# Kernel tuning notes

Measured on AMD Instinct MI355X. Metric: run time of the kernel, lower is better.

## Reference

```python
import jax, jax.numpy as jnp
import numpy as np

B = 64        # number of bags
D = 512       # feature dim
T = 131072    # total instances across all bags (ragged, avg ~2048/bag)


def setup_inputs() -> dict:
    key = jax.random.key(0)
    k_s, _ = jax.random.split(key)
    samples = jax.random.normal(k_s, (T, D), dtype=jnp.float32)
    # Ragged bag sizes that sum exactly to T (deterministic).
    rng = np.random.default_rng(0)
    w = rng.random(B)
    counts = np.floor(w / w.sum() * T).astype(np.int64)
    counts = np.maximum(counts, 1)
    counts[-1] += T - counts.sum()
    bags_num_samples = jnp.asarray(counts, dtype=jnp.int64)
    return {"samples": samples, "bags_num_samples": bags_num_samples}


def reference(samples, bags_num_samples):
    # Fused segmented mean-pool replacing the per-bag Python loop:
    # bag i owns rows [cum[i-1], cum[i]) of `samples`.
    n_bags = bags_num_samples.shape[0]
    total = samples.shape[0]
    seg_ids = jnp.repeat(jnp.arange(n_bags), bags_num_samples,
                         total_repeat_length=total)  # [T]
    sums = jax.ops.segment_sum(samples, seg_ids, num_segments=n_bags)  # [B, D]
    return sums / bags_num_samples[:, None].astype(samples.dtype)
```

## Files before the change

kernel.cpp:

```cpp
#include <hip/hip_runtime.h>

#define NBAGS 64
#define D 512
#define D4 128
#define TARGET_CHUNKS 1024
#define GRID1 1088


__device__ __forceinline__ int lane_incl_scan(int v, int lane) {
#pragma unroll
    for (int off = 1; off < 64; off <<= 1) {
        int o = __shfl_up(v, off, 64);
        if (lane >= off) v += o;
    }
    return v;
}

__global__ __launch_bounds__(256) void
agg_partial_kernel(const float* __restrict__ samples,
                   const int* __restrict__ counts,
                   float* __restrict__ partials, int tt) {
    __shared__ int s_bag, s_r0, s_r1;
    const int t = threadIdx.x;
    const int g = blockIdx.x;

    if (t == 0) s_bag = -1;
    if (t < 64) {
        const int c = counts[t];
        int n = (c * TARGET_CHUNKS) / tt;
        if (n < 1) n = 1;
        int S = n;
#pragma unroll
        for (int m = 1; m < 64; m <<= 1) S += __shfl_xor(S, m, 64);
        int L = TARGET_CHUNKS - S; if (L < 0) L = 0;
        n += (t < L) ? 1 : 0;
        const int cb = lane_incl_scan(n, t) - n;
        const int rb = lane_incl_scan(c, t) - c;
        if (g >= cb && g < cb + n) {
            const int j = g - cb;
            s_bag = t;
            s_r0 = rb + (c * j) / n;
            s_r1 = rb + (c * (j + 1)) / n;
        }
    }
    __syncthreads();
    if (s_bag < 0) return;
    const int r0 = s_r0, r1 = s_r1;

    const int col  = t & (D4 - 1);
    const int half = t >> 7;

    const float4* __restrict__ src = (const float4*)samples;

    float4 a0 = make_float4(0.f, 0.f, 0.f, 0.f);
    float4 a1 = make_float4(0.f, 0.f, 0.f, 0.f);
    int r = r0 + half;
    for (; r + 6 < r1; r += 8) {
        float4 v0 = src[(r    ) * D4 + col];
        float4 v1 = src[(r + 2) * D4 + col];
        float4 v2 = src[(r + 4) * D4 + col];
        float4 v3 = src[(r + 6) * D4 + col];
        a0.x += v0.x; a0.y += v0.y; a0.z += v0.z; a0.w += v0.w;
        a1.x += v1.x; a1.y += v1.y; a1.z += v1.z; a1.w += v1.w;
        a0.x += v2.x; a0.y += v2.y; a0.z += v2.z; a0.w += v2.w;
        a1.x += v3.x; a1.y += v3.y; a1.z += v3.z; a1.w += v3.w;
    }
    for (; r < r1; r += 2) {
        float4 v = src[r * D4 + col];
        a0.x += v.x; a0.y += v.y; a0.z += v.z; a0.w += v.w;
    }
    a0.x += a1.x; a0.y += a1.y; a0.z += a1.z; a0.w += a1.w;

    __shared__ float4 lds[D4];
    if (half == 1) lds[col] = a0;
    __syncthreads();
    if (half == 0) {
        float4 o = lds[col];
        a0.x += o.x; a0.y += o.y; a0.z += o.z; a0.w += o.w;
        ((float4*)partials)[g * D4 + col] = a0;
    }
}

__global__ __launch_bounds__(D4) void
agg_reduce_kernel(const float* __restrict__ partials,
                  const int* __restrict__ counts,
                  float* __restrict__ out, int tt) {
    __shared__ int s_cb, s_n;
    const int t   = threadIdx.x;
    const int bag = blockIdx.x;

    if (t < 64) {
        const int c = counts[t];
        int n = (c * TARGET_CHUNKS) / tt;
        if (n < 1) n = 1;
        int S = n;
#pragma unroll
        for (int m = 1; m < 64; m <<= 1) S += __shfl_xor(S, m, 64);
        int L = TARGET_CHUNKS - S; if (L < 0) L = 0;
        n += (t < L) ? 1 : 0;
        const int cb = lane_incl_scan(n, t) - n;
        if (t == bag) { s_cb = cb; s_n = n; }
    }
    __syncthreads();
    const int cb = s_cb, n = s_n;

    const float4* __restrict__ p = (const float4*)partials;
    float4 acc = make_float4(0.f, 0.f, 0.f, 0.f);
    for (int k = 0; k < n; ++k) {
        float4 v = p[(cb + k) * D4 + t];
        acc.x += v.x; acc.y += v.y; acc.z += v.z; acc.w += v.w;
    }
    const float inv = 1.0f / (float)counts[bag];
    acc.x *= inv; acc.y *= inv; acc.z *= inv; acc.w *= inv;
    ((float4*)out)[bag * D4 + t] = acc;
}

extern "C" void kernel_launch(void* const* d_in, const int* in_sizes, int n_in,
                              void* d_out, int out_size, void* d_ws, size_t ws_size,
                              hipStream_t stream) {
    const float* samples  = (const float*)d_in[0];
    const int*   counts   = (const int*)d_in[1];
    float*       out      = (float*)d_out;
    float*       partials = (float*)d_ws;
    const int    tt       = in_sizes[0] / D;

    agg_partial_kernel<<<GRID1, 256, 0, stream>>>(samples, counts, partials, tt);
    agg_reduce_kernel<<<NBAGS, D4, 0, stream>>>(partials, counts, out, tt);
}
```

Measured before the change: 56.21 us.

## Fuse partial and reduce kernels using atomicAdd into zeroed output

Drops the second reduction kernel and the partials workspace. Each chunk block now scales its partial sum by 1/count and atomically adds it into the output, which is zeroed first with hipMemsetAsync. This removes one kernel launch and the partials write/read round trip, at the cost of float atomics, a memset launch, and non-deterministic summation order.

```diff
diff --git a/kernel.cpp b/kernel.cpp
--- a/kernel.cpp
+++ b/kernel.cpp
@@ -17,10 +17,10 @@
 }
 
 __global__ __launch_bounds__(256) void
-agg_partial_kernel(const float* __restrict__ samples,
-                   const int* __restrict__ counts,
-                   float* __restrict__ partials, int tt) {
-    __shared__ int s_bag, s_r0, s_r1;
+agg_fused_kernel(const float* __restrict__ samples,
+                 const int* __restrict__ counts,
+                 float* __restrict__ out, int tt) {
+    __shared__ int s_bag, s_r0, s_r1, s_cnt;
     const int t = threadIdx.x;
     const int g = blockIdx.x;
 
@@ -39,6 +39,7 @@
         if (g >= cb && g < cb + n) {
             const int j = g - cb;
             s_bag = t;
+            s_cnt = c;
             s_r0 = rb + (c * j) / n;
             s_r1 = rb + (c * (j + 1)) / n;
         }
@@ -77,53 +78,23 @@
     if (half == 0) {
         float4 o = lds[col];
         a0.x += o.x; a0.y += o.y; a0.z += o.z; a0.w += o.w;
-        ((float4*)partials)[g * D4 + col] = a0;
+        const float inv = 1.0f / (float)s_cnt;
+        float* dst = out + s_bag * D + col * 4;
+        atomicAdd(dst + 0, a0.x * inv);
+        atomicAdd(dst + 1, a0.y * inv);
+        atomicAdd(dst + 2, a0.z * inv);
+        atomicAdd(dst + 3, a0.w * inv);
     }
-}
-
-__global__ __launch_bounds__(D4) void
-agg_reduce_kernel(const float* __restrict__ partials,
-                  const int* __restrict__ counts,
-                  float* __restrict__ out, int tt) {
-    __shared__ int s_cb, s_n;
-    const int t   = threadIdx.x;
-    const int bag = blockIdx.x;
-
-    if (t < 64) {
-        const int c = counts[t];
-        int n = (c * TARGET_CHUNKS) / tt;
-        if (n < 1) n = 1;
-        int S = n;
-#pragma unroll
-        for (int m = 1; m < 64; m <<= 1) S += __shfl_xor(S, m, 64);
-        int L = TARGET_CHUNKS - S; if (L < 0) L = 0;
-        n += (t < L) ? 1 : 0;
-        const int cb = lane_incl_scan(n, t) - n;
-        if (t == bag) { s_cb = cb; s_n = n; }
-    }
-    __syncthreads();
-    const int cb = s_cb, n = s_n;
-
-    const float4* __restrict__ p = (const float4*)partials;
-    float4 acc = make_float4(0.f, 0.f, 0.f, 0.f);
-    for (int k = 0; k < n; ++k) {
-        float4 v = p[(cb + k) * D4 + t];
-        acc.x += v.x; acc.y += v.y; acc.z += v.z; acc.w += v.w;
-    }
-    const float inv = 1.0f / (float)counts[bag];
-    acc.x *= inv; acc.y *= inv; acc.z *= inv; acc.w *= inv;
-    ((float4*)out)[bag * D4 + t] = acc;
 }
 
 extern "C" void kernel_launch(void* const* d_in, const int* in_sizes, int n_in,
                               void* d_out, int out_size, void* d_ws, size_t ws_size,
                               hipStream_t stream) {
-    const float* samples  = (const float*)d_in[0];
-    const int*   counts   = (const int*)d_in[1];
-    float*       out      = (float*)d_out;
-    float*       partials = (float*)d_ws;
-    const int    tt       = in_sizes[0] / D;
+    const float* samples = (const float*)d_in[0];
+    const int*   counts  = (const int*)d_in[1];
+    float*       out     = (float*)d_out;
+    const int    tt      = in_sizes[0] / D;
 
-    agg_partial_kernel<<<GRID1, 256, 0, stream>>>(samples, counts, partials, tt);
-    agg_reduce_kernel<<<NBAGS, D4, 0, stream>>>(partials, counts, out, tt);
+    hipMemsetAsync(out, 0, (size_t)out_size * sizeof(float), stream);
+    agg_fused_kernel<<<GRID1, 256, 0, stream>>>(samples, counts, out, tt);
 }
```

New measurement: 54.00 us. 3.9% less time.
